# Kernel tuning notes

Measured on AMD Instinct MI355X. Metric: run time of the kernel, lower is better.

## Reference

```python
import jax, jax.numpy as jnp
import numpy as np

S, B, L = 512, 256, 128  # seq_length, batch_size, label_nums
PAD_ID, START_ID = 0, 1


def setup_inputs() -> dict:
    key = jax.random.key(0)
    k1, k2, k3, k4 = jax.random.split(key, 4)
    emit_scores = jax.random.normal(k1, (S, B, L), dtype=jnp.float32)
    labels = jax.random.randint(k2, (B, S), 0, L, dtype=jnp.int32)
    # contiguous prefix masks: lengths in [1, S]
    lengths = jax.random.randint(k3, (B,), 1, S + 1, dtype=jnp.int32)
    masks = jnp.arange(S, dtype=jnp.int32)[None, :] < lengths[:, None]  # (B, S) bool
    T = jax.random.normal(k4, (L, L), dtype=jnp.float32) * 0.1  # transition params
    return {"emit_scores": emit_scores, "labels": labels, "masks": masks, "T": T}


def reference(emit_scores, labels, masks, T):
    seq_len, batch, label_nums = emit_scores.shape

    # ---- gold path score (calc_sentences_scores) ----
    lengths = masks.astype(jnp.int32).sum(axis=1)                       # (B,)
    ends_index = jnp.take_along_axis(labels, (lengths - 1)[:, None], axis=1)[:, 0]
    ends_scores = T[ends_index, PAD_ID].sum()

    labels_ext = jnp.concatenate(
        [jnp.full((batch, 1), START_ID, dtype=labels.dtype), labels], axis=1)  # (B, S+1)
    prev = labels_ext[:, :-1]                                           # (B, S)
    nxt = labels                                                        # (B, S)
    emit_bt = jnp.transpose(emit_scores, (1, 0, 2))                     # (B, S, L)
    emit_sel = jnp.take_along_axis(emit_bt, nxt[:, :, None], axis=2)[:, :, 0]  # (B, S)
    trans_sel = T[prev, nxt]                                            # (B, S)
    gold = jnp.where(masks, emit_sel + trans_sel, 0.0).sum() + ends_scores

    # ---- partition function (crf_encode): log-sum-exp scan over time ----
    fs0 = emit_scores[0] + T[START_ID][None, :]                         # (B, L)

    def step(fs, inp):
        e_t, m_t = inp                                                  # (B, L), (B,)
        # scores[b, i, j] = fs[b, i] + T[i, j] + e_t[b, j]
        scores = fs[:, :, None] + T[None, :, :] + e_t[:, None, :]
        cur = jax.nn.logsumexp(scores, axis=1)                          # (B, L)
        fs = jnp.where(m_t[:, None], cur, fs)
        return fs, None

    fs, _ = jax.lax.scan(step, fs0, (emit_scores[1:], masks.T[1:]))
    encode = jax.nn.logsumexp(fs + T[:, PAD_ID][None, :], axis=1).sum()

    return encode - gold
```

## Files before the change

kernel.cpp:

```cpp
#include <hip/hip_runtime.h>
#include <hip/hip_fp8.h>

#define S_LEN 512
#define BATCH 256
#define L 128
#define PAD_ID 0
#define START_ID 1

typedef int    i32x8 __attribute__((ext_vector_type(8)));
typedef int    i32x4 __attribute__((ext_vector_type(4)));
typedef float  f32x4 __attribute__((ext_vector_type(4)));
typedef unsigned int   u32x4 __attribute__((ext_vector_type(4)));
typedef unsigned short u16x2 __attribute__((ext_vector_type(2)));

__device__ __forceinline__ unsigned int umax2(unsigned int a, unsigned int b) {
    u16x2 x = __builtin_bit_cast(u16x2, a), y = __builtin_bit_cast(u16x2, b);
#if defined(__has_builtin) && __has_builtin(__builtin_elementwise_max)
    return __builtin_bit_cast(unsigned int, __builtin_elementwise_max(x, y));
#else
    u16x2 r; r.x = x.x > y.x ? x.x : y.x; r.y = x.y > y.y ? x.y : y.y;
    return __builtin_bit_cast(unsigned int, r);
#endif
}
__device__ __forceinline__ float frcp(float x) {
#if defined(__has_builtin) && __has_builtin(__builtin_amdgcn_rcpf)
    return __builtin_amdgcn_rcpf(x);
#else
    return 1.0f / x;
#endif
}
__device__ __forceinline__ unsigned short f2bf(float f) {
    unsigned int u = __builtin_bit_cast(unsigned int, f);
    return (unsigned short)((u + 0x7fffu + ((u >> 16) & 1u)) >> 16);
}
__device__ __forceinline__ float bf2f(unsigned short b) {
    return __builtin_bit_cast(float, (unsigned int)b << 16);
}
__device__ __forceinline__ float sane(float x, float lo, float hi) {
    return fminf(fmaxf(x, lo), hi);
}
__device__ __forceinline__ int pk2_fp8(float a, float b) {
#if defined(__has_builtin) && __has_builtin(__builtin_amdgcn_cvt_pk_fp8_f32)
    return __builtin_amdgcn_cvt_pk_fp8_f32(a, b, 0, false);
#else
    __hip_fp8_e4m3 A(a), B(b);
    return (int)A.__x | ((int)B.__x << 8);
#endif
}
__device__ __forceinline__ unsigned int bmax8(u32x4 a, u32x4 b) {
    const unsigned int M = 0x00FF00FFu;
    unsigned int l0 = umax2(a.x & M, a.y & M), l1 = umax2(a.z & M, a.w & M);
    unsigned int l2 = umax2(b.x & M, b.y & M), l3 = umax2(b.z & M, b.w & M);
    unsigned int h0 = umax2((a.x >> 8) & M, (a.y >> 8) & M);
    unsigned int h1 = umax2((a.z >> 8) & M, (a.w >> 8) & M);
    unsigned int h2 = umax2((b.x >> 8) & M, (b.y >> 8) & M);
    unsigned int h3 = umax2((b.z >> 8) & M, (b.w >> 8) & M);
    unsigned int v = umax2(umax2(umax2(l0, l1), umax2(l2, l3)),
                           umax2(umax2(h0, h1), umax2(h2, h3)));
    u16x2 t = __builtin_bit_cast(u16x2, v);
    return (unsigned int)(t.x > t.y ? t.x : t.y);
}
__device__ __forceinline__ float fp8dec(unsigned int bb) {
    bb &= 0x7Fu;
    int e = (int)(bb >> 3), mt = (int)(bb & 7u);
    float v = e ? __builtin_ldexpf((float)(8 + mt), e - 10)
                : __builtin_ldexpf((float)mt, -9);
    return sane(v, 1e-9f, 448.f);
}

__global__ __launch_bounds__(512, 1) void k_scan(
        const float* __restrict__ emit, const int* __restrict__ labels,
        const void* __restrict__ masks, const float* __restrict__ T,
        float* __restrict__ out) {
    const int b = blockIdx.x;
    const int tid = threadIdx.x;
    const int w = tid >> 6;
    const int dir = w >> 2;
    const int wl = w & 3;
    const int lane = tid & 63;
    const int g = lane >> 4, m = lane & 15;
    const int ja = 32 * wl + m, jb = ja + 16;

    __shared__ unsigned short elds[512][L];
    __shared__ __align__(16) unsigned char qs[2][2][L];
    __shared__ __align__(16) unsigned char hb[2][2][4];
    __shared__ float part[12];
    __shared__ float fsx[8];
    __shared__ float Ssh[2];
    __shared__ int   ib[8];

    {
        const unsigned int* mw0 = (const unsigned int*)masks;
        int pred = 0;
        #pragma unroll
        for (int k = 0; k < 4; ++k) {
            unsigned int w0 = mw0[tid + 512 * k];
            pred |= (w0 > 1u && w0 != 0x3f800000u);
        }
        unsigned long long bal = __ballot(pred);
        if (lane == 0) ib[w] = (bal != 0ull) ? 1 : 0;
        if (tid < 16)  ((unsigned char*)hb)[tid] = 0x38;
        if (tid < 512) ((unsigned char*)qs)[tid] = 0x38;
        if (tid < 12)  part[tid] = 0.f;
        if (tid < 8)   fsx[tid] = 0.f;
        if (tid < 2)   Ssh[tid] = 0.f;
    }
    __syncthreads();
    const bool isbyte = (ib[0] | ib[1] | ib[2] | ib[3] | ib[4] | ib[5] | ib[6] | ib[7]) != 0;

    int len;
    {
        int cnt = 0;
        if (isbyte) {
            const unsigned int* mw = (const unsigned int*)masks + b * (S_LEN / 4);
            #pragma unroll
            for (int k = 0; k < 2; ++k) {
                unsigned int w0 = mw[lane + 64 * k];
                cnt += ((w0 & 0xffu) != 0) + ((w0 & 0xff00u) != 0) +
                       ((w0 & 0xff0000u) != 0) + ((w0 & 0xff000000u) != 0);
            }
        } else {
            const unsigned int* mw = (const unsigned int*)masks + b * S_LEN;
            #pragma unroll
            for (int k = 0; k < 8; ++k) cnt += (mw[lane + 64 * k] != 0u);
        }
        #pragma unroll
        for (int off = 32; off; off >>= 1) cnt += __shfl_xor(cnt, off, 64);
        len = cnt;
    }
    const int n  = len - 1;
    const int kf = n / 2;
    const int nB = n - kf - 1;

#define LDBX(BF, nt, TR)                                                                     \
    {                                                                                        \
        _Pragma("unroll")                                                                    \
        for (int d = 0; d < 8; ++d) {                                                        \
            int s0 = 32 * g + 4 * d;                                                         \
            float v0, v1, v2, v3;                                                            \
            if (TR) {                                                                        \
                v0 = __expf(T[(16 * (nt) + m) * L + (16 * ((s0 + 0) & 7) + ((s0 + 0) >> 3))]); \
                v1 = __expf(T[(16 * (nt) + m) * L + (16 * ((s0 + 1) & 7) + ((s0 + 1) >> 3))]); \
                v2 = __expf(T[(16 * (nt) + m) * L + (16 * ((s0 + 2) & 7) + ((s0 + 2) >> 3))]); \
                v3 = __expf(T[(16 * (nt) + m) * L + (16 * ((s0 + 3) & 7) + ((s0 + 3) >> 3))]); \
            } else {                                                                         \
                v0 = __expf(T[(16 * ((s0 + 0) & 7) + ((s0 + 0) >> 3)) * L + 16 * (nt) + m]);   \
                v1 = __expf(T[(16 * ((s0 + 1) & 7) + ((s0 + 1) >> 3)) * L + 16 * (nt) + m]);   \
                v2 = __expf(T[(16 * ((s0 + 2) & 7) + ((s0 + 2) >> 3)) * L + 16 * (nt) + m]);   \
                v3 = __expf(T[(16 * ((s0 + 3) & 7) + ((s0 + 3) >> 3)) * L + 16 * (nt) + m]);   \
            }                                                                                \
            int p01 = pk2_fp8(v0, v1), p23 = pk2_fp8(v2, v3);                                \
            BF[d] = (p01 & 0xffff) | (p23 << 16);                                            \
        }                                                                                    \
    }
    i32x8 Bq0, Bq1;
    if (dir == 0) { LDBX(Bq0, 2 * wl, 0) LDBX(Bq1, 2 * wl + 1, 0) }
    else          { LDBX(Bq0, 2 * wl, 1) LDBX(Bq1, 2 * wl + 1, 1) }

    const float eTpa = T[ja * L + PAD_ID];
    const float eTpb = T[jb * L + PAD_ID];

    for (int idx = tid; idx < n * 64; idx += 512) {
        int r = 1 + (idx >> 6), c2 = (idx & 63) * 2;
        const float* ep = emit + ((size_t)r * BATCH + b) * L + c2;
        float e0 = ep[0], e1 = ep[1];
        *(unsigned int*)&elds[r][c2] =
            (unsigned int)f2bf(e0) | ((unsigned int)f2bf(e1) << 16);
    }
    __syncthreads();

    float fa = 0.f, fbv = 0.f;
    if (dir == 0) {
        fa  = emit[b * L + ja] + T[START_ID * L + ja];
        fbv = emit[b * L + jb] + T[START_ID * L + jb];
    } else if (n >= 1) {
        fa  = emit[((size_t)n * BATCH + b) * L + ja] + eTpa;
        fbv = emit[((size_t)n * BATCH + b) * L + jb] + eTpb;
    }
    {
        float mx = fmaxf(fa, fbv);
        #pragma unroll
        for (int off = 32; off; off >>= 1) mx = fmaxf(mx, __shfl_xor(mx, off, 64));
        if (lane == 0) fsx[w] = mx;
    }
    __syncthreads();
    float S = 0.f, p0 = 0.f, p1 = 0.f;
    if (dir == 0 || n >= 1) {
        S = dir ? fmaxf(fmaxf(fsx[4], fsx[5]), fmaxf(fsx[6], fsx[7]))
                : fmaxf(fmaxf(fsx[0], fsx[1]), fmaxf(fsx[2], fsx[3]));
        p0 = sane(__expf(fa - S), 1e-9f, 400.f);
        p1 = sane(__expf(fbv - S), 1e-9f, 400.f);
        if (g == 0)
            *(short*)&qs[dir][0][8 * m + 2 * wl] = (short)(pk2_fp8(p0, p1) & 0xffff);
    }
    __syncthreads();

    const f32x4 z = {0.f, 0.f, 0.f, 0.f};
    for (int i = 0; i < kf; ++i) {
        bool act = dir ? (i < nB) : true;
        if (act) {
            const int rb = i & 1, wb2 = (i + 1) & 1;
            const int row = dir ? (n - 1 - i) : (i + 1);

            i32x4 alo = *(const i32x4*)&qs[dir][rb][32 * g];
            i32x4 ahi = *(const i32x4*)&qs[dir][rb][32 * g + 16];
            unsigned int hd = *(const unsigned int*)&hb[dir][rb][0];
            float ea = bf2f(elds[row][ja]);
            float eb = bf2f(elds[row][jb]);
            float xe0 = __expf(ea), xe1 = __expf(eb);

            {
                const unsigned int M = 0x00FF00FFu;
                unsigned int v = umax2(hd & M, (hd >> 8) & M);
                u16x2 tv = __builtin_bit_cast(u16x2, v);
                hd = (unsigned int)(tv.x > tv.y ? tv.x : tv.y);
            }
            float msc = fp8dec(hd);
            float kk = frcp(msc);

            i32x8 A;
            A[0] = alo[0]; A[1] = alo[1]; A[2] = alo[2]; A[3] = alo[3];
            A[4] = ahi[0]; A[5] = ahi[1]; A[6] = ahi[2]; A[7] = ahi[3];

            f32x4 c0 = __builtin_amdgcn_mfma_scale_f32_16x16x128_f8f6f4(A, Bq0, z, 0, 0, 0, 127, 0, 127);
            f32x4 c1 = __builtin_amdgcn_mfma_scale_f32_16x16x128_f8f6f4(A, Bq1, z, 0, 0, 0, 127, 0, 127);

            unsigned int qm = bmax8(__builtin_bit_cast(u32x4, alo),
                                    __builtin_bit_cast(u32x4, ahi));
            if (wl == 0 && m == 0) hb[dir][wb2][g] = (unsigned char)(qm & 0x7Fu);

            p0 = sane(c0[0] * kk * xe0, 1e-9f, 400.f);
            p1 = sane(c1[0] * kk * xe1, 1e-9f, 400.f);
            if (g == 0)
                *(short*)&qs[dir][wb2][8 * m + 2 * wl] = (short)(pk2_fp8(p0, p1) & 0xffff);
            S += __logf(msc);
        }
        __syncthreads();
    }

    float ev = 0.f;
    if (n >= 1) {
        if (dir == 0) {
            const int rb = kf & 1, bufB = nB & 1;
            i32x4 alo = *(const i32x4*)&qs[0][rb][32 * g];
            i32x4 ahi = *(const i32x4*)&qs[0][rb][32 * g + 16];
            i32x8 A;
            A[0] = alo[0]; A[1] = alo[1]; A[2] = alo[2]; A[3] = alo[3];
            A[4] = ahi[0]; A[5] = ahi[1]; A[6] = ahi[2]; A[7] = ahi[3];
            f32x4 c0 = __builtin_amdgcn_mfma_scale_f32_16x16x128_f8f6f4(A, Bq0, z, 0, 0, 0, 127, 0, 127);
            f32x4 c1 = __builtin_amdgcn_mfma_scale_f32_16x16x128_f8f6f4(A, Bq1, z, 0, 0, 0, 127, 0, 127);
            if (g == 0) {
                float ua = fp8dec(qs[1][bufB][8 * m + 2 * wl]);
                float ub = fp8dec(qs[1][bufB][8 * m + 2 * wl + 1]);
                ev = sane(c0[0], 0.f, 3e7f) * ua + sane(c1[0], 0.f, 3e7f) * ub;
            }
        }
    } else {
        if (dir == 0 && g == 0) ev = p0 * __expf(eTpa) + p1 * __expf(eTpb);
    }
    #pragma unroll
    for (int off = 32; off; off >>= 1) ev += __shfl_xor(ev, off, 64);
    if (dir == 0 && lane == 0) part[wl] = ev;
    if (tid == 0) Ssh[0] = S;
    if (w == 4 && lane == 0 && n >= 1) Ssh[1] = S;

    float gsum = 0.f;
    for (int tt = tid; tt < len; tt += 512) {
        int nxt = labels[b * S_LEN + tt];
        int prv = tt ? labels[b * S_LEN + tt - 1] : START_ID;
        gsum += emit[((size_t)tt * BATCH + b) * L + nxt] + T[prv * L + nxt];
        if (tt == len - 1) gsum += T[nxt * L + PAD_ID];
    }
    #pragma unroll
    for (int off = 32; off; off >>= 1) gsum += __shfl_xor(gsum, off, 64);
    if (lane == 0) part[4 + w] = gsum;
    __syncthreads();

    if (tid == 0) {
        float evs = fmaxf((part[0] + part[1]) + (part[2] + part[3]), 1e-35f);
        float enc  = Ssh[0] + Ssh[1] + __logf(evs);
        float gold = ((part[4] + part[5]) + (part[6] + part[7])) +
                     ((part[8] + part[9]) + (part[10] + part[11]));
        float contrib = sane(enc - gold, -1e30f, 1e30f);
        atomicAdd(out, contrib);
    }
}

extern "C" void kernel_launch(void* const* d_in, const int* in_sizes, int n_in,
                              void* d_out, int out_size, void* d_ws, size_t ws_size,
                              hipStream_t stream) {
    const float* emit   = (const float*)d_in[0];
    const int*   labels = (const int*)d_in[1];
    const void*  masks  = d_in[2];
    const float* T      = (const float*)d_in[3];
    float* out = (float*)d_out;

    hipMemsetAsync(d_out, 0, sizeof(float), stream);
    k_scan<<<dim3(BATCH), dim3(512), 0, stream>>>(emit, labels, masks, T, out);
}
```

Measured before the change: 234.8 us.

## Split forward/backward CRF scans into separate blocks with a join kernel

The forward and backward halves of the log-sum-exp scan, previously run by two wave groups inside one 512-thread block per batch element, now run as separate 256-thread blocks (512 blocks total). Each block stages only its own half of the emissions in LDS, which halves LDS use and drops the dead-iteration predicate. The fp8 seam vectors and running log-scales go to the workspace, and a second small kernel combines them with a scalar T-exp dot product. This doubles block count to fill more CUs and shortens per-block barrier loops, at the cost of an extra launch and workspace round trip.

```diff
diff --git a/kernel.cpp b/kernel.cpp
--- a/kernel.cpp
+++ b/kernel.cpp
@@ -68,45 +68,47 @@
     return sane(v, 1e-9f, 448.f);
 }
 
-__global__ __launch_bounds__(512, 1) void k_scan(
+#define WS_QF 0
+#define WS_QB 32768
+#define WS_SF 65536
+#define WS_SB 66560
+#define WS_N  67584
+
+__global__ __launch_bounds__(256, 1) void k_scan2(
         const float* __restrict__ emit, const int* __restrict__ labels,
         const void* __restrict__ masks, const float* __restrict__ T,
-        float* __restrict__ out) {
-    const int b = blockIdx.x;
+        unsigned char* __restrict__ ws, float* __restrict__ out) {
+    const int b   = blockIdx.x & (BATCH - 1);
+    const int dir = blockIdx.x >> 8;
     const int tid = threadIdx.x;
     const int w = tid >> 6;
-    const int dir = w >> 2;
-    const int wl = w & 3;
     const int lane = tid & 63;
     const int g = lane >> 4, m = lane & 15;
-    const int ja = 32 * wl + m, jb = ja + 16;
-
-    __shared__ unsigned short elds[512][L];
-    __shared__ __align__(16) unsigned char qs[2][2][L];
-    __shared__ __align__(16) unsigned char hb[2][2][4];
-    __shared__ float part[12];
-    __shared__ float fsx[8];
-    __shared__ float Ssh[2];
-    __shared__ int   ib[8];
+    const int ja = 32 * w + m, jb = ja + 16;
+
+    __shared__ unsigned short elds[255][L];
+    __shared__ __align__(16) unsigned char qs[2][L];
+    __shared__ __align__(8)  unsigned char hb[2][4];
+    __shared__ float part[4];
+    __shared__ float fsx[4];
+    __shared__ int   ib[4];
 
     {
         const unsigned int* mw0 = (const unsigned int*)masks;
         int pred = 0;
         #pragma unroll
-        for (int k = 0; k < 4; ++k) {
-            unsigned int w0 = mw0[tid + 512 * k];
+        for (int k = 0; k < 8; ++k) {
+            unsigned int w0 = mw0[tid + 256 * k];
             pred |= (w0 > 1u && w0 != 0x3f800000u);
         }
         unsigned long long bal = __ballot(pred);
         if (lane == 0) ib[w] = (bal != 0ull) ? 1 : 0;
-        if (tid < 16)  ((unsigned char*)hb)[tid] = 0x38;
-        if (tid < 512) ((unsigned char*)qs)[tid] = 0x38;
-        if (tid < 12)  part[tid] = 0.f;
-        if (tid < 8)   fsx[tid] = 0.f;
-        if (tid < 2)   Ssh[tid] = 0.f;
+        if (tid < 8)   ((unsigned char*)hb)[tid] = 0x38;
+        if (tid < 256) ((unsigned char*)qs)[tid] = 0x38;
+        if (tid < 4)   { part[tid] = 0.f; fsx[tid] = 0.f; }
     }
     __syncthreads();
-    const bool isbyte = (ib[0] | ib[1] | ib[2] | ib[3] | ib[4] | ib[5] | ib[6] | ib[7]) != 0;
+    const bool isbyte = (ib[0] | ib[1] | ib[2] | ib[3]) != 0;
 
     int len;
     {
@@ -131,6 +133,7 @@
     const int n  = len - 1;
     const int kf = n / 2;
     const int nB = n - kf - 1;
+    const int steps = dir ? (nB > 0 ? nB : 0) : kf;
 
 #define LDBX(BF, nt, TR)                                                                     \
     {                                                                                        \
@@ -154,28 +157,26 @@
         }                                                                                    \
     }
     i32x8 Bq0, Bq1;
-    if (dir == 0) { LDBX(Bq0, 2 * wl, 0) LDBX(Bq1, 2 * wl + 1, 0) }
-    else          { LDBX(Bq0, 2 * wl, 1) LDBX(Bq1, 2 * wl + 1, 1) }
-
-    const float eTpa = T[ja * L + PAD_ID];
-    const float eTpb = T[jb * L + PAD_ID];
-
-    for (int idx = tid; idx < n * 64; idx += 512) {
-        int r = 1 + (idx >> 6), c2 = (idx & 63) * 2;
-        const float* ep = emit + ((size_t)r * BATCH + b) * L + c2;
+    if (dir == 0) { LDBX(Bq0, 2 * w, 0) LDBX(Bq1, 2 * w + 1, 0) }
+    else          { LDBX(Bq0, 2 * w, 1) LDBX(Bq1, 2 * w + 1, 1) }
+
+    for (int idx = tid; idx < steps * 64; idx += 256) {
+        int rl = idx >> 6, c2 = (idx & 63) * 2;
+        int row = dir ? (kf + 1 + rl) : (1 + rl);
+        const float* ep = emit + ((size_t)row * BATCH + b) * L + c2;
         float e0 = ep[0], e1 = ep[1];
-        *(unsigned int*)&elds[r][c2] =
+        *(unsigned int*)&elds[rl][c2] =
             (unsigned int)f2bf(e0) | ((unsigned int)f2bf(e1) << 16);
     }
-    __syncthreads();
 
     float fa = 0.f, fbv = 0.f;
+    const bool active = (dir == 0) || (n >= 1);
     if (dir == 0) {
         fa  = emit[b * L + ja] + T[START_ID * L + ja];
         fbv = emit[b * L + jb] + T[START_ID * L + jb];
     } else if (n >= 1) {
-        fa  = emit[((size_t)n * BATCH + b) * L + ja] + eTpa;
-        fbv = emit[((size_t)n * BATCH + b) * L + jb] + eTpb;
+        fa  = emit[((size_t)n * BATCH + b) * L + ja] + T[ja * L + PAD_ID];
+        fbv = emit[((size_t)n * BATCH + b) * L + jb] + T[jb * L + PAD_ID];
     }
     {
         float mx = fmaxf(fa, fbv);
@@ -185,104 +186,121 @@
     }
     __syncthreads();
     float S = 0.f, p0 = 0.f, p1 = 0.f;
-    if (dir == 0 || n >= 1) {
-        S = dir ? fmaxf(fmaxf(fsx[4], fsx[5]), fmaxf(fsx[6], fsx[7]))
-                : fmaxf(fmaxf(fsx[0], fsx[1]), fmaxf(fsx[2], fsx[3]));
+    if (active) {
+        S = fmaxf(fmaxf(fsx[0], fsx[1]), fmaxf(fsx[2], fsx[3]));
         p0 = sane(__expf(fa - S), 1e-9f, 400.f);
         p1 = sane(__expf(fbv - S), 1e-9f, 400.f);
         if (g == 0)
-            *(short*)&qs[dir][0][8 * m + 2 * wl] = (short)(pk2_fp8(p0, p1) & 0xffff);
+            *(short*)&qs[0][8 * m + 2 * w] = (short)(pk2_fp8(p0, p1) & 0xffff);
     }
     __syncthreads();
 
     const f32x4 z = {0.f, 0.f, 0.f, 0.f};
-    for (int i = 0; i < kf; ++i) {
-        bool act = dir ? (i < nB) : true;
-        if (act) {
-            const int rb = i & 1, wb2 = (i + 1) & 1;
-            const int row = dir ? (n - 1 - i) : (i + 1);
-
-            i32x4 alo = *(const i32x4*)&qs[dir][rb][32 * g];
-            i32x4 ahi = *(const i32x4*)&qs[dir][rb][32 * g + 16];
-            unsigned int hd = *(const unsigned int*)&hb[dir][rb][0];
-            float ea = bf2f(elds[row][ja]);
-            float eb = bf2f(elds[row][jb]);
-            float xe0 = __expf(ea), xe1 = __expf(eb);
-
-            {
-                const unsigned int M = 0x00FF00FFu;
-                unsigned int v = umax2(hd & M, (hd >> 8) & M);
-                u16x2 tv = __builtin_bit_cast(u16x2, v);
-                hd = (unsigned int)(tv.x > tv.y ? tv.x : tv.y);
-            }
-            float msc = fp8dec(hd);
-            float kk = frcp(msc);
-
-            i32x8 A;
-            A[0] = alo[0]; A[1] = alo[1]; A[2] = alo[2]; A[3] = alo[3];
-            A[4] = ahi[0]; A[5] = ahi[1]; A[6] = ahi[2]; A[7] = ahi[3];
-
-            f32x4 c0 = __builtin_amdgcn_mfma_scale_f32_16x16x128_f8f6f4(A, Bq0, z, 0, 0, 0, 127, 0, 127);
-            f32x4 c1 = __builtin_amdgcn_mfma_scale_f32_16x16x128_f8f6f4(A, Bq1, z, 0, 0, 0, 127, 0, 127);
-
-            unsigned int qm = bmax8(__builtin_bit_cast(u32x4, alo),
-                                    __builtin_bit_cast(u32x4, ahi));
-            if (wl == 0 && m == 0) hb[dir][wb2][g] = (unsigned char)(qm & 0x7Fu);
-
-            p0 = sane(c0[0] * kk * xe0, 1e-9f, 400.f);
-            p1 = sane(c1[0] * kk * xe1, 1e-9f, 400.f);
-            if (g == 0)
-                *(short*)&qs[dir][wb2][8 * m + 2 * wl] = (short)(pk2_fp8(p0, p1) & 0xffff);
-            S += __logf(msc);
-        }
+    for (int i = 0; i < steps; ++i) {
+        const int rb = i & 1, wb2 = (i + 1) & 1;
+        const int slot = dir ? (nB - 1 - i) : i;
+
+        i32x4 alo = *(const i32x4*)&qs[rb][32 * g];
+        i32x4 ahi = *(const i32x4*)&qs[rb][32 * g + 16];
+        unsigned int hd = *(const unsigned int*)&hb[rb][0];
+        float ea = bf2f(elds[slot][ja]);
+        float eb = bf2f(elds[slot][jb]);
+        float xe0 = __expf(ea), xe1 = __expf(eb);
+
+        {
+            const unsigned int M = 0x00FF00FFu;
+            unsigned int v = umax2(hd & M, (hd >> 8) & M);
+            u16x2 tv = __builtin_bit_cast(u16x2, v);
+            hd = (unsigned int)(tv.x > tv.y ? tv.x : tv.y);
+        }
+        float msc = fp8dec(hd);
+        float kk = frcp(msc);
+
+        i32x8 A;
+        A[0] = alo[0]; A[1] = alo[1]; A[2] = alo[2]; A[3] = alo[3];
+        A[4] = ahi[0]; A[5] = ahi[1]; A[6] = ahi[2]; A[7] = ahi[3];
+
+        f32x4 c0 = __builtin_amdgcn_mfma_scale_f32_16x16x128_f8f6f4(A, Bq0, z, 0, 0, 0, 127, 0, 127);
+        f32x4 c1 = __builtin_amdgcn_mfma_scale_f32_16x16x128_f8f6f4(A, Bq1, z, 0, 0, 0, 127, 0, 127);
+
+        unsigned int qm = bmax8(__builtin_bit_cast(u32x4, alo),
+                                __builtin_bit_cast(u32x4, ahi));
+        if (w == 0 && m == 0) hb[wb2][g] = (unsigned char)(qm & 0x7Fu);
+
+        p0 = sane(c0[0] * kk * xe0, 1e-9f, 400.f);
+        p1 = sane(c1[0] * kk * xe1, 1e-9f, 400.f);
+        if (g == 0)
+            *(short*)&qs[wb2][8 * m + 2 * w] = (short)(pk2_fp8(p0, p1) & 0xffff);
+        S += __logf(msc);
         __syncthreads();
     }
+
+    unsigned char* seam = ws + (dir ? WS_QB : WS_QF) + b * L;
+    if (tid < 32) ((int*)seam)[tid] = ((const int*)qs[steps & 1])[tid];
+    if (tid == 0) {
+        ((float*)(ws + (dir ? WS_SB : WS_SF)))[b] = S;
+        if (dir == 0) ((int*)(ws + WS_N))[b] = n;
+    }
+
+    if (dir == 0) {
+        float gsum = 0.f;
+        for (int tt = tid; tt < len; tt += 256) {
+            int nxt = labels[b * S_LEN + tt];
+            int prv = tt ? labels[b * S_LEN + tt - 1] : START_ID;
+            gsum += emit[((size_t)tt * BATCH + b) * L + nxt] + T[prv * L + nxt];
+            if (tt == len - 1) gsum += T[nxt * L + PAD_ID];
+        }
+        #pragma unroll
+        for (int off = 32; off; off >>= 1) gsum += __shfl_xor(gsum, off, 64);
+        if (lane == 0) part[w] = gsum;
+        __syncthreads();
+        if (tid == 0)
+            atomicAdd(out, -((part[0] + part[1]) + (part[2] + part[3])));
+    }
+}
+
+__global__ __launch_bounds__(64, 1) void k_join(
+        const float* __restrict__ T, const unsigned char* __restrict__ ws,
+        float* __restrict__ out) {
+    const int b = blockIdx.x;
+    const int lane = threadIdx.x;
+    __shared__ float qsh[L], ush[L];
+
+    const int n = ((const int*)(ws + WS_N))[b];
+    #pragma unroll
+    for (int k = 0; k < 2; ++k) {
+        int s = lane + 64 * k;
+        int j = 16 * (s & 7) + (s >> 3);
+        qsh[j] = fp8dec(ws[WS_QF + b * L + s]);
+        ush[j] = fp8dec(ws[WS_QB + b * L + s]);
+    }
+    __syncthreads();
 
     float ev = 0.f;
     if (n >= 1) {
-        if (dir == 0) {
-            const int rb = kf & 1, bufB = nB & 1;
-            i32x4 alo = *(const i32x4*)&qs[0][rb][32 * g];
-            i32x4 ahi = *(const i32x4*)&qs[0][rb][32 * g + 16];
-            i32x8 A;
-            A[0] = alo[0]; A[1] = alo[1]; A[2] = alo[2]; A[3] = alo[3];
-            A[4] = ahi[0]; A[5] = ahi[1]; A[6] = ahi[2]; A[7] = ahi[3];
-            f32x4 c0 = __builtin_amdgcn_mfma_scale_f32_16x16x128_f8f6f4(A, Bq0, z, 0, 0, 0, 127, 0, 127);
-            f32x4 c1 = __builtin_amdgcn_mfma_scale_f32_16x16x128_f8f6f4(A, Bq1, z, 0, 0, 0, 127, 0, 127);
-            if (g == 0) {
-                float ua = fp8dec(qs[1][bufB][8 * m + 2 * wl]);
-                float ub = fp8dec(qs[1][bufB][8 * m + 2 * wl + 1]);
-                ev = sane(c0[0], 0.f, 3e7f) * ua + sane(c1[0], 0.f, 3e7f) * ub;
-            }
+        #pragma unroll
+        for (int k = 0; k < 2; ++k) {
+            int j = lane + 64 * k;
+            float v = 0.f;
+            for (int i = 0; i < L; ++i)
+                v = fmaf(qsh[i], __expf(T[i * L + j]), v);
+            ev += v * ush[j];
         }
     } else {
-        if (dir == 0 && g == 0) ev = p0 * __expf(eTpa) + p1 * __expf(eTpb);
+        #pragma unroll
+        for (int k = 0; k < 2; ++k) {
+            int j = lane + 64 * k;
+            ev += qsh[j] * __expf(T[j * L + PAD_ID]);
+        }
     }
     #pragma unroll
     for (int off = 32; off; off >>= 1) ev += __shfl_xor(ev, off, 64);
-    if (dir == 0 && lane == 0) part[wl] = ev;
-    if (tid == 0) Ssh[0] = S;
-    if (w == 4 && lane == 0 && n >= 1) Ssh[1] = S;
-
-    float gsum = 0.f;
-    for (int tt = tid; tt < len; tt += 512) {
-        int nxt = labels[b * S_LEN + tt];
-        int prv = tt ? labels[b * S_LEN + tt - 1] : START_ID;
-        gsum += emit[((size_t)tt * BATCH + b) * L + nxt] + T[prv * L + nxt];
-        if (tt == len - 1) gsum += T[nxt * L + PAD_ID];
-    }
-    #pragma unroll
-    for (int off = 32; off; off >>= 1) gsum += __shfl_xor(gsum, off, 64);
-    if (lane == 0) part[4 + w] = gsum;
-    __syncthreads();
-
-    if (tid == 0) {
-        float evs = fmaxf((part[0] + part[1]) + (part[2] + part[3]), 1e-35f);
-        float enc  = Ssh[0] + Ssh[1] + __logf(evs);
-        float gold = ((part[4] + part[5]) + (part[6] + part[7])) +
-                     ((part[8] + part[9]) + (part[10] + part[11]));
-        float contrib = sane(enc - gold, -1e30f, 1e30f);
-        atomicAdd(out, contrib);
+
+    if (lane == 0) {
+        float Sf = ((const float*)(ws + WS_SF))[b];
+        float Sb = (n >= 1) ? ((const float*)(ws + WS_SB))[b] : 0.f;
+        float enc = Sf + Sb + __logf(fmaxf(ev, 1e-35f));
+        atomicAdd(out, sane(enc, -1e30f, 1e30f));
     }
 }
 
@@ -294,7 +312,9 @@
     const void*  masks  = d_in[2];
     const float* T      = (const float*)d_in[3];
     float* out = (float*)d_out;
+    unsigned char* ws = (unsigned char*)d_ws;
 
     hipMemsetAsync(d_out, 0, sizeof(float), stream);
-    k_scan<<<dim3(BATCH), dim3(512), 0, stream>>>(emit, labels, masks, T, out);
-}
+    k_scan2<<<dim3(2 * BATCH), dim3(256), 0, stream>>>(emit, labels, masks, T, ws, out);
+    k_join <<<dim3(BATCH),     dim3(64),  0, stream>>>(T, ws, out);
+}
```

New measurement: 227.9 us. -3.0%, faster.
